# Optimization experiments

Measured on AMD Instinct MI355X. Metric: run time of the kernel, lower is better.

Reference implementation:

```python
import jax, jax.numpy as jnp
import numpy as np

VIS_DIM = 4096
HIDDEN_D = 4096
EMB_DIM = 512
B = 128
N_NEG = 2048


def setup_inputs() -> dict:
    key = jax.random.key(0)
    k = jax.random.split(key, 7)
    vfs = jax.random.normal(k[0], (B, VIS_DIM), dtype=jnp.float32)
    p_lfs = jax.random.normal(k[1], (B, EMB_DIM), dtype=jnp.float32)
    n_lfs = jax.random.normal(k[2], (N_NEG, EMB_DIM), dtype=jnp.float32)
    # Linear params (PyTorch layout: W [out, in], y = x @ W.T + b)
    s_h = 1.0 / np.sqrt(VIS_DIM)
    s_e = 1.0 / np.sqrt(HIDDEN_D)
    W_h = jax.random.uniform(k[3], (HIDDEN_D, VIS_DIM), jnp.float32, -s_h, s_h)
    b_h = jax.random.uniform(k[4], (HIDDEN_D,), jnp.float32, -s_h, s_h)
    W_e = jax.random.uniform(k[5], (EMB_DIM, HIDDEN_D), jnp.float32, -s_e, s_e)
    b_e = jax.random.uniform(k[6], (EMB_DIM,), jnp.float32, -s_e, s_e)
    return {"vfs": vfs, "p_lfs": p_lfs, "n_lfs": n_lfs,
            "W_h": W_h, "b_h": b_h, "W_e": W_e, "b_e": b_e}


def _partial_order_sim(hypers, hypos):
    # -||relu(hypers - hypos)||_2 reduced over the last axis
    act = jax.nn.relu(hypers - hypos)
    return -jnp.sqrt(jnp.sum(act * act, axis=-1))


def reference(vfs, p_lfs, n_lfs, W_h, b_h, W_e, b_e):
    # Two plain Linears (NO ReLU in between, matching the original forward)
    vf_hidden = vfs @ W_h.T + b_h            # [B, 4096]
    vf_emb = vf_hidden @ W_e.T + b_e          # [B, emb]
    # positive score per sample
    p_scores = _partial_order_sim(p_lfs, vf_emb)                    # [B]
    # negative scores, batched over all samples at once (replaces per-sample loop)
    n_scores = _partial_order_sim(n_lfs[None, :, :], vf_emb[:, None, :])  # [B, N]
    score_stack = jnp.concatenate([p_scores[:, None], n_scores], axis=1)  # [B, N+1]
    return score_stack
```

## Files before the change

### kernel.cpp

```cpp
#include <hip/hip_runtime.h>

#define B_N  128
#define VIS  4096
#define HID  4096
#define EMB  512
#define NNEG 2048
#define OUTN (NNEG + 1)

using f32x4  = __attribute__((ext_vector_type(4))) float;
using bf16x8 = __attribute__((ext_vector_type(8))) short;

static __device__ __forceinline__ unsigned short f2bf(float f) {
  unsigned u = __builtin_bit_cast(unsigned, f);
  u += 0x7fffu + ((u >> 16) & 1u);
  return (unsigned short)(u >> 16);
}

union U16x8 { unsigned short us[8]; uint4 v; };
union U16x4 { unsigned short us[4]; uint2 v; };
union U16x2 { unsigned short us[2]; unsigned v; };

#define PIPE_BARRIER() __asm__ volatile("s_waitcnt lgkmcnt(0)\n\ts_barrier" ::: "memory")

__global__ __launch_bounds__(256) void prep_kernel(
    const float* __restrict__ src, unsigned short* __restrict__ dst,
    float* __restrict__ emb) {
  const int idx = blockIdx.x * 256 + threadIdx.x;
  float4 a = ((const float4*)src)[idx * 2];
  float4 b = ((const float4*)src)[idx * 2 + 1];
  U16x8 pk;
  pk.us[0] = f2bf(a.x); pk.us[1] = f2bf(a.y); pk.us[2] = f2bf(a.z); pk.us[3] = f2bf(a.w);
  pk.us[4] = f2bf(b.x); pk.us[5] = f2bf(b.y); pk.us[6] = f2bf(b.z); pk.us[7] = f2bf(b.w);
  ((uint4*)dst)[idx] = pk.v;
  if (idx < (B_N * EMB / 4))
    ((float4*)emb)[idx] = make_float4(0.f, 0.f, 0.f, 0.f);
}

__global__ __launch_bounds__(512, 4) void gemm1_kernel(
    const unsigned short* __restrict__ Abf, const float* __restrict__ Wh,
    const float* __restrict__ bh, float* __restrict__ Hp) {
  const int n0    = blockIdx.x * 32;
  const int kbase = blockIdx.y * 1024;

  __shared__ __align__(16) unsigned short Ws[2][32 * 64];

  const int t = threadIdx.x, w = t >> 6, lane = t & 63;
  const int m_lane = lane & 15, kq = lane >> 4;
  f32x4 acc[2] = {};

  const int wr = t >> 4, Gw = (t & 15) >> 1, sub = (t & 1) * 4;
  const float* Wg = Wh + (size_t)(n0 + wr) * VIS + kbase + (t & 15) * 4;
  const int wofs = wr * 64 + ((Gw ^ (wr & 7)) * 8) + sub;

  const int arow = w * 16 + m_lane;
  const unsigned short* Ag = Abf + (size_t)arow * VIS + kbase + kq * 8;

  float4 wv[3];
  bf16x8 av[3][2];

  wv[0] = *(const float4*)(Wg);
  wv[1] = *(const float4*)(Wg + 64);
  wv[2] = *(const float4*)(Wg + 128);
  av[0][0] = *(const bf16x8*)(Ag);
  av[0][1] = *(const bf16x8*)(Ag + 32);
  av[1][0] = *(const bf16x8*)(Ag + 64);
  av[1][1] = *(const bf16x8*)(Ag + 96);
  {
    U16x4 pk;
    pk.us[0] = f2bf(wv[0].x); pk.us[1] = f2bf(wv[0].y);
    pk.us[2] = f2bf(wv[0].z); pk.us[3] = f2bf(wv[0].w);
    *(uint2*)&Ws[0][wofs] = pk.v;
  }
  PIPE_BARRIER();

#pragma unroll
  for (int k = 0; k < 16; ++k) {
    const int cur = k & 1;
    if (k + 3 < 16) wv[k % 3] = *(const float4*)(Wg + (k + 3) * 64);
    if (k + 2 < 16) {
      av[(k + 2) % 3][0] = *(const bf16x8*)(Ag + (k + 2) * 64);
      av[(k + 2) % 3][1] = *(const bf16x8*)(Ag + (k + 2) * 64 + 32);
    }
    if (k + 1 < 16) {
      const float4 wc = wv[(k + 1) % 3];
      U16x4 pk;
      pk.us[0] = f2bf(wc.x); pk.us[1] = f2bf(wc.y);
      pk.us[2] = f2bf(wc.z); pk.us[3] = f2bf(wc.w);
      *(uint2*)&Ws[1 - cur][wofs] = pk.v;
    }
#pragma unroll
    for (int ks = 0; ks < 2; ++ks) {
      const int Gk = ks * 4 + kq;
      const int cA = m_lane, cB = m_lane + 16;
      bf16x8 b0 = *(const bf16x8*)&Ws[cur][cA * 64 + ((Gk ^ (cA & 7)) * 8)];
      bf16x8 b1 = *(const bf16x8*)&Ws[cur][cB * 64 + ((Gk ^ (cB & 7)) * 8)];
      acc[0] = __builtin_amdgcn_mfma_f32_16x16x32_bf16(av[k % 3][ks], b0, acc[0], 0, 0, 0);
      acc[1] = __builtin_amdgcn_mfma_f32_16x16x32_bf16(av[k % 3][ks], b1, acc[1], 0, 0, 0);
    }
    PIPE_BARRIER();
  }

  float* Pd = Hp + (size_t)blockIdx.y * (B_N * HID);
  const int rq = (lane >> 4) * 4;
#pragma unroll
  for (int ni = 0; ni < 2; ++ni) {
    const int ng = n0 + ni * 16 + m_lane;
    const float bias = (blockIdx.y == 0) ? bh[ng] : 0.0f;
#pragma unroll
    for (int r = 0; r < 4; ++r)
      Pd[(size_t)(w * 16 + rq + r) * HID + ng] = acc[ni][r] + bias;
  }
}

__global__ __launch_bounds__(256) void cvt_kernel(
    const float* __restrict__ Hp, unsigned short* __restrict__ dst) {
  const int idx = blockIdx.x * 256 + threadIdx.x;
  const size_t PS = (size_t)B_N * HID;
  float4 a = ((const float4*)Hp)[idx * 2];
  float4 b = ((const float4*)Hp)[idx * 2 + 1];
#pragma unroll
  for (int p = 1; p < 4; ++p) {
    float4 ap = ((const float4*)(Hp + p * PS))[idx * 2];
    float4 bp = ((const float4*)(Hp + p * PS))[idx * 2 + 1];
    a.x += ap.x; a.y += ap.y; a.z += ap.z; a.w += ap.w;
    b.x += bp.x; b.y += bp.y; b.z += bp.z; b.w += bp.w;
  }
  U16x8 pk;
  pk.us[0] = f2bf(a.x); pk.us[1] = f2bf(a.y); pk.us[2] = f2bf(a.z); pk.us[3] = f2bf(a.w);
  pk.us[4] = f2bf(b.x); pk.us[5] = f2bf(b.y); pk.us[6] = f2bf(b.z); pk.us[7] = f2bf(b.w);
  ((uint4*)dst)[idx] = pk.v;
}

__global__ __launch_bounds__(512, 4) void gemm2_kernel(
    const unsigned short* __restrict__ Hbf, const float* __restrict__ We,
    const float* __restrict__ be, float* __restrict__ emb) {
  const int n0    = blockIdx.x * 16;
  const int kbase = blockIdx.y * 512;

  __shared__ __align__(16) unsigned short Ws[2][16 * 64];

  const int t = threadIdx.x, w = t >> 6, lane = t & 63;
  const int m_lane = lane & 15, kq = lane >> 4;
  f32x4 acc = {};

  const int wr = t >> 5, e = (t & 31) * 2;
  const float* Wg = We + (size_t)(n0 + wr) * HID + kbase + e;
  const int wofs = wr * 64 + (((e >> 3) ^ (wr & 7)) * 8) + (e & 7);

  const int arow = w * 16 + m_lane;
  const unsigned short* Ag = Hbf + (size_t)arow * HID + kbase + kq * 8;

  float2 wv[3];
  bf16x8 av[3][2];

  wv[0] = *(const float2*)(Wg);
  wv[1] = *(const float2*)(Wg + 64);
  wv[2] = *(const float2*)(Wg + 128);
  av[0][0] = *(const bf16x8*)(Ag);
  av[0][1] = *(const bf16x8*)(Ag + 32);
  av[1][0] = *(const bf16x8*)(Ag + 64);
  av[1][1] = *(const bf16x8*)(Ag + 96);
  {
    U16x2 pk;
    pk.us[0] = f2bf(wv[0].x); pk.us[1] = f2bf(wv[0].y);
    *(unsigned*)&Ws[0][wofs] = pk.v;
  }
  PIPE_BARRIER();

#pragma unroll
  for (int k = 0; k < 8; ++k) {
    const int cur = k & 1;
    if (k + 3 < 8) wv[k % 3] = *(const float2*)(Wg + (k + 3) * 64);
    if (k + 2 < 8) {
      av[(k + 2) % 3][0] = *(const bf16x8*)(Ag + (k + 2) * 64);
      av[(k + 2) % 3][1] = *(const bf16x8*)(Ag + (k + 2) * 64 + 32);
    }
    if (k + 1 < 8) {
      const float2 wc = wv[(k + 1) % 3];
      U16x2 pk;
      pk.us[0] = f2bf(wc.x); pk.us[1] = f2bf(wc.y);
      *(unsigned*)&Ws[1 - cur][wofs] = pk.v;
    }
#pragma unroll
    for (int ks = 0; ks < 2; ++ks) {
      const int Gk = ks * 4 + kq;
      bf16x8 b0 = *(const bf16x8*)&Ws[cur][m_lane * 64 + ((Gk ^ (m_lane & 7)) * 8)];
      acc = __builtin_amdgcn_mfma_f32_16x16x32_bf16(av[k % 3][ks], b0, acc, 0, 0, 0);
    }
    PIPE_BARRIER();
  }

  const int rq = (lane >> 4) * 4;
  const int ng = n0 + m_lane;
  const float bias = (blockIdx.y == 0) ? be[ng] : 0.0f;
#pragma unroll
  for (int r = 0; r < 4; ++r)
    atomicAdd(&emb[(w * 16 + rq + r) * EMB + ng], acc[r] + bias);
}

__global__ __launch_bounds__(256, 2) void score_kernel(
    const float* __restrict__ emb, const float* __restrict__ n_lfs,
    const float* __restrict__ p_lfs, float* __restrict__ out) {
  const int bx = blockIdx.x;
  const int t = threadIdx.x;
  const int s = t & 15, tb = t >> 4;

  if (bx < 1024) {
    const int nc = bx >> 3, bt = bx & 7;
    const int n0 = nc * 16, b0 = bt * 16;
    __shared__ __align__(16) float nl[16 * 576];
#pragma unroll
    for (int i = 0; i < 8; ++i) {
      const int f = t + i * 256;
      const int r = f >> 7, o4 = f & 127;
      float4 v = *(const float4*)(n_lfs + (size_t)(n0 + r) * EMB + o4 * 4);
      *(float4*)&nl[r * 576 + (o4 >> 3) * 36 + (o4 & 7) * 4] = v;
    }
    const float* eb = emb + (size_t)(b0 + tb) * EMB + s * 32;
    float4 ev[8];
#pragma unroll
    for (int i = 0; i < 8; ++i) ev[i] = *(const float4*)(eb + i * 4);
    __syncthreads();

    for (int j = 0; j < 16; ++j) {
      const float* nr = &nl[j * 576 + s * 36];
      float a0 = 0.f, a1 = 0.f, a2 = 0.f, a3 = 0.f;
#pragma unroll
      for (int i = 0; i < 8; ++i) {
        float4 nv = *(const float4*)(nr + i * 4);
        float d0 = fmaxf(nv.x - ev[i].x, 0.f);
        float d1 = fmaxf(nv.y - ev[i].y, 0.f);
        float d2 = fmaxf(nv.z - ev[i].z, 0.f);
        float d3 = fmaxf(nv.w - ev[i].w, 0.f);
        a0 = fmaf(d0, d0, a0); a1 = fmaf(d1, d1, a1);
        a2 = fmaf(d2, d2, a2); a3 = fmaf(d3, d3, a3);
      }
      float ss = (a0 + a1) + (a2 + a3);
      ss += __shfl_xor(ss, 1);
      ss += __shfl_xor(ss, 2);
      ss += __shfl_xor(ss, 4);
      ss += __shfl_xor(ss, 8);
      if (s == 0) out[(size_t)(b0 + tb) * OUTN + 1 + n0 + j] = -sqrtf(ss);
    }
  } else {
    const int b = (bx - 1024) * 16 + tb;
    const float* eb = emb + (size_t)b * EMB + s * 32;
    const float* pb = p_lfs + (size_t)b * EMB + s * 32;
    float a0 = 0.f, a1 = 0.f, a2 = 0.f, a3 = 0.f;
#pragma unroll
    for (int i = 0; i < 8; ++i) {
      float4 pv = *(const float4*)(pb + i * 4);
      float4 ev = *(const float4*)(eb + i * 4);
      float d0 = fmaxf(pv.x - ev.x, 0.f);
      float d1 = fmaxf(pv.y - ev.y, 0.f);
      float d2 = fmaxf(pv.z - ev.z, 0.f);
      float d3 = fmaxf(pv.w - ev.w, 0.f);
      a0 = fmaf(d0, d0, a0); a1 = fmaf(d1, d1, a1);
      a2 = fmaf(d2, d2, a2); a3 = fmaf(d3, d3, a3);
    }
    float ss = (a0 + a1) + (a2 + a3);
    ss += __shfl_xor(ss, 1);
    ss += __shfl_xor(ss, 2);
    ss += __shfl_xor(ss, 4);
    ss += __shfl_xor(ss, 8);
    if (s == 0) out[(size_t)b * OUTN] = -sqrtf(ss);
  }
}

extern "C" void kernel_launch(void* const* d_in, const int* in_sizes, int n_in,
                              void* d_out, int out_size, void* d_ws, size_t ws_size,
                              hipStream_t stream) {
  const float* vfs   = (const float*)d_in[0];
  const float* p_lfs = (const float*)d_in[1];
  const float* n_lfs = (const float*)d_in[2];
  const float* W_h   = (const float*)d_in[3];
  const float* b_h   = (const float*)d_in[4];
  const float* W_e   = (const float*)d_in[5];
  const float* b_e   = (const float*)d_in[6];
  float* out = (float*)d_out;

  char* ws = (char*)d_ws;
  float*          Hp  = (float*)ws;
  float*          emb = (float*)(ws + (8u << 20));
  unsigned short* Abf = (unsigned short*)(ws + (8u << 20) + (256u << 10));
  unsigned short* Hbf = (unsigned short*)(ws + (9u << 20) + (256u << 10));

  prep_kernel<<<256, 256, 0, stream>>>(vfs, Abf, emb);
  gemm1_kernel<<<dim3(HID / 32, 4), 512, 0, stream>>>(Abf, W_h, b_h, Hp);
  cvt_kernel<<<256, 256, 0, stream>>>(Hp, Hbf);
  gemm2_kernel<<<dim3(EMB / 16, 8), 512, 0, stream>>>(Hbf, W_e, b_e, emb);
  score_kernel<<<1032, 256, 0, stream>>>(emb, n_lfs, p_lfs, out);
}
```

Baseline: 160.1 us.

## Raise gemm1 split-K to 8 and use packed bf16 conversion intrinsic

The first GEMM's split-K factor goes from 4 to 8, so the grid doubles to 1024 blocks and each block covers half the K range. The workspace layout is enlarged to hold 8 fp32 partial buffers, and cvt_kernel now sums 8 partials. The hand-written bf16 rounding is replaced by the HIP __float22bfloat162_rn packed conversion. More blocks should fill the GPU better and hide latency, but this doubles partial-sum write and read traffic (16MB of fp32 partials).

Measured after the change: 162.7 us. About the same (+1.6%).

```diff
diff --git a/kernel.cpp b/kernel.cpp
--- a/kernel.cpp
+++ b/kernel.cpp
@@ -1,4 +1,5 @@
 #include <hip/hip_runtime.h>
+#include <hip/hip_bf16.h>
 
 #define B_N  128
 #define VIS  4096
@@ -6,19 +7,16 @@
 #define EMB  512
 #define NNEG 2048
 #define OUTN (NNEG + 1)
+#define SPLIT1 8
 
 using f32x4  = __attribute__((ext_vector_type(4))) float;
 using bf16x8 = __attribute__((ext_vector_type(8))) short;
 
-static __device__ __forceinline__ unsigned short f2bf(float f) {
-  unsigned u = __builtin_bit_cast(unsigned, f);
-  u += 0x7fffu + ((u >> 16) & 1u);
-  return (unsigned short)(u >> 16);
-}
-
-union U16x8 { unsigned short us[8]; uint4 v; };
-union U16x4 { unsigned short us[4]; uint2 v; };
-union U16x2 { unsigned short us[2]; unsigned v; };
+static __device__ __forceinline__ unsigned pk2bf(float x, float y) {
+  union { __hip_bfloat162 h; unsigned u; } c;
+  c.h = __float22bfloat162_rn(make_float2(x, y));
+  return c.u;
+}
 
 #define PIPE_BARRIER() __asm__ volatile("s_waitcnt lgkmcnt(0)\n\ts_barrier" ::: "memory")
 
@@ -28,10 +26,10 @@
   const int idx = blockIdx.x * 256 + threadIdx.x;
   float4 a = ((const float4*)src)[idx * 2];
   float4 b = ((const float4*)src)[idx * 2 + 1];
-  U16x8 pk;
-  pk.us[0] = f2bf(a.x); pk.us[1] = f2bf(a.y); pk.us[2] = f2bf(a.z); pk.us[3] = f2bf(a.w);
-  pk.us[4] = f2bf(b.x); pk.us[5] = f2bf(b.y); pk.us[6] = f2bf(b.z); pk.us[7] = f2bf(b.w);
-  ((uint4*)dst)[idx] = pk.v;
+  uint4 pk;
+  pk.x = pk2bf(a.x, a.y); pk.y = pk2bf(a.z, a.w);
+  pk.z = pk2bf(b.x, b.y); pk.w = pk2bf(b.z, b.w);
+  ((uint4*)dst)[idx] = pk;
   if (idx < (B_N * EMB / 4))
     ((float4*)emb)[idx] = make_float4(0.f, 0.f, 0.f, 0.f);
 }
@@ -40,7 +38,7 @@
     const unsigned short* __restrict__ Abf, const float* __restrict__ Wh,
     const float* __restrict__ bh, float* __restrict__ Hp) {
   const int n0    = blockIdx.x * 32;
-  const int kbase = blockIdx.y * 1024;
+  const int kbase = blockIdx.y * 512;
 
   __shared__ __align__(16) unsigned short Ws[2][32 * 64];
 
@@ -52,8 +50,7 @@
   const float* Wg = Wh + (size_t)(n0 + wr) * VIS + kbase + (t & 15) * 4;
   const int wofs = wr * 64 + ((Gw ^ (wr & 7)) * 8) + sub;
 
-  const int arow = w * 16 + m_lane;
-  const unsigned short* Ag = Abf + (size_t)arow * VIS + kbase + kq * 8;
+  const unsigned short* Ag = Abf + (size_t)(w * 16 + m_lane) * VIS + kbase + kq * 8;
 
   float4 wv[3];
   bf16x8 av[3][2];
@@ -66,27 +63,23 @@
   av[1][0] = *(const bf16x8*)(Ag + 64);
   av[1][1] = *(const bf16x8*)(Ag + 96);
   {
-    U16x4 pk;
-    pk.us[0] = f2bf(wv[0].x); pk.us[1] = f2bf(wv[0].y);
-    pk.us[2] = f2bf(wv[0].z); pk.us[3] = f2bf(wv[0].w);
-    *(uint2*)&Ws[0][wofs] = pk.v;
+    uint2 pk = make_uint2(pk2bf(wv[0].x, wv[0].y), pk2bf(wv[0].z, wv[0].w));
+    *(uint2*)&Ws[0][wofs] = pk;
   }
   PIPE_BARRIER();
 
 #pragma unroll
-  for (int k = 0; k < 16; ++k) {
+  for (int k = 0; k < 8; ++k) {
     const int cur = k & 1;
-    if (k + 3 < 16) wv[k % 3] = *(const float4*)(Wg + (k + 3) * 64);
-    if (k + 2 < 16) {
+    if (k + 3 < 8) wv[k % 3] = *(const float4*)(Wg + (k + 3) * 64);
+    if (k + 2 < 8) {
       av[(k + 2) % 3][0] = *(const bf16x8*)(Ag + (k + 2) * 64);
       av[(k + 2) % 3][1] = *(const bf16x8*)(Ag + (k + 2) * 64 + 32);
     }
-    if (k + 1 < 16) {
+    if (k + 1 < 8) {
       const float4 wc = wv[(k + 1) % 3];
-      U16x4 pk;
-      pk.us[0] = f2bf(wc.x); pk.us[1] = f2bf(wc.y);
-      pk.us[2] = f2bf(wc.z); pk.us[3] = f2bf(wc.w);
-      *(uint2*)&Ws[1 - cur][wofs] = pk.v;
+      uint2 pk = make_uint2(pk2bf(wc.x, wc.y), pk2bf(wc.z, wc.w));
+      *(uint2*)&Ws[1 - cur][wofs] = pk;
     }
 #pragma unroll
     for (int ks = 0; ks < 2; ++ks) {
@@ -119,16 +112,16 @@
   float4 a = ((const float4*)Hp)[idx * 2];
   float4 b = ((const float4*)Hp)[idx * 2 + 1];
 #pragma unroll
-  for (int p = 1; p < 4; ++p) {
+  for (int p = 1; p < SPLIT1; ++p) {
     float4 ap = ((const float4*)(Hp + p * PS))[idx * 2];
     float4 bp = ((const float4*)(Hp + p * PS))[idx * 2 + 1];
     a.x += ap.x; a.y += ap.y; a.z += ap.z; a.w += ap.w;
     b.x += bp.x; b.y += bp.y; b.z += bp.z; b.w += bp.w;
   }
-  U16x8 pk;
-  pk.us[0] = f2bf(a.x); pk.us[1] = f2bf(a.y); pk.us[2] = f2bf(a.z); pk.us[3] = f2bf(a.w);
-  pk.us[4] = f2bf(b.x); pk.us[5] = f2bf(b.y); pk.us[6] = f2bf(b.z); pk.us[7] = f2bf(b.w);
-  ((uint4*)dst)[idx] = pk.v;
+  uint4 pk;
+  pk.x = pk2bf(a.x, a.y); pk.y = pk2bf(a.z, a.w);
+  pk.z = pk2bf(b.x, b.y); pk.w = pk2bf(b.z, b.w);
+  ((uint4*)dst)[idx] = pk;
 }
 
 __global__ __launch_bounds__(512, 4) void gemm2_kernel(
@@ -147,8 +140,7 @@
   const float* Wg = We + (size_t)(n0 + wr) * HID + kbase + e;
   const int wofs = wr * 64 + (((e >> 3) ^ (wr & 7)) * 8) + (e & 7);
 
-  const int arow = w * 16 + m_lane;
-  const unsigned short* Ag = Hbf + (size_t)arow * HID + kbase + kq * 8;
+  const unsigned short* Ag = Hbf + (size_t)(w * 16 + m_lane) * HID + kbase + kq * 8;
 
   float2 wv[3];
   bf16x8 av[3][2];
@@ -160,11 +152,7 @@
   av[0][1] = *(const bf16x8*)(Ag + 32);
   av[1][0] = *(const bf16x8*)(Ag + 64);
   av[1][1] = *(const bf16x8*)(Ag + 96);
-  {
-    U16x2 pk;
-    pk.us[0] = f2bf(wv[0].x); pk.us[1] = f2bf(wv[0].y);
-    *(unsigned*)&Ws[0][wofs] = pk.v;
-  }
+  *(unsigned*)&Ws[0][wofs] = pk2bf(wv[0].x, wv[0].y);
   PIPE_BARRIER();
 
 #pragma unroll
@@ -177,9 +165,7 @@
     }
     if (k + 1 < 8) {
       const float2 wc = wv[(k + 1) % 3];
-      U16x2 pk;
-      pk.us[0] = f2bf(wc.x); pk.us[1] = f2bf(wc.y);
-      *(unsigned*)&Ws[1 - cur][wofs] = pk.v;
+      *(unsigned*)&Ws[1 - cur][wofs] = pk2bf(wc.x, wc.y);
     }
 #pragma unroll
     for (int ks = 0; ks < 2; ++ks) {
@@ -281,12 +267,12 @@
 
   char* ws = (char*)d_ws;
   float*          Hp  = (float*)ws;
-  float*          emb = (float*)(ws + (8u << 20));
-  unsigned short* Abf = (unsigned short*)(ws + (8u << 20) + (256u << 10));
-  unsigned short* Hbf = (unsigned short*)(ws + (9u << 20) + (256u << 10));
+  float*          emb = (float*)(ws + (16u << 20));
+  unsigned short* Abf = (unsigned short*)(ws + (16u << 20) + (256u << 10));
+  unsigned short* Hbf = (unsigned short*)(ws + (17u << 20) + (256u << 10));
 
   prep_kernel<<<256, 256, 0, stream>>>(vfs, Abf, emb);
-  gemm1_kernel<<<dim3(HID / 32, 4), 512, 0, stream>>>(Abf, W_h, b_h, Hp);
+  gemm1_kernel<<<dim3(HID / 32, SPLIT1), 512, 0, stream>>>(Abf, W_h, b_h, Hp);
   cvt_kernel<<<256, 256, 0, stream>>>(Hp, Hbf);
   gemm2_kernel<<<dim3(EMB / 16, 8), 512, 0, stream>>>(Hbf, W_e, b_e, emb);
   score_kernel<<<1032, 256, 0, stream>>>(emb, n_lfs, p_lfs, out);
```
